# Performance work log

Hardware: AMD Instinct MI355X
Metric: run time of the kernel (lower is better)

## Reference

```python
import jax, jax.numpy as jnp
import numpy as np

FEAT = 256          # feat_channels == point_feat_channels == in_channels
STACK = 3           # stacked_convs
NPTS = 9            # num_points -> dcn_kernel = 3
NCLS = 80           # num_classes
GM = 0.1            # gradient_mul
GROUPS = 32         # 32 * 256 // 256
EPS = 1e-5
BIAS_CLS = -float(np.log((1 - 0.01) / 0.01))  # prior_prob focal-bias init


def conv2d(x, w, b=None):
    y = jax.lax.conv_general_dilated(x, w, (1, 1), 'SAME',
                                     dimension_numbers=('NCHW', 'OIHW', 'NCHW'))
    return y if b is None else y + b[None, :, None, None]


def group_norm(x, w, b):
    B, C, H, W = x.shape
    xg = x.reshape(B, GROUPS, C // GROUPS, H, W)
    mu = xg.mean((2, 3, 4), keepdims=True)
    var = xg.var((2, 3, 4), keepdims=True)
    xn = ((xg - mu) * jax.lax.rsqrt(var + EPS)).reshape(B, C, H, W)
    return xn * w[None, :, None, None] + b[None, :, None, None]


def bilinear_sample(x, py, px):
    # x: [B,C,H,W]; py,px: [B,K,H,W] absolute sample coords -> [B,C,K,H,W]
    B, C, H, W = x.shape
    y0 = jnp.floor(py); x0 = jnp.floor(px)
    wy = (py - y0)[:, None]; wx = (px - x0)[:, None]  # [B,1,K,H,W]
    xf = x.reshape(B, C, H * W)

    def gather(yi, xi):
        valid = (yi >= 0) & (yi < H) & (xi >= 0) & (xi < W)
        yic = jnp.clip(yi, 0, H - 1).astype(jnp.int32)
        xic = jnp.clip(xi, 0, W - 1).astype(jnp.int32)
        idx = (yic * W + xic).reshape(B, -1)                       # [B,K*H*W]
        g = jax.vmap(lambda xb, ib: xb[:, ib])(xf, idx)            # [B,C,K*H*W]
        g = g.reshape(B, C, *yi.shape[1:])
        return g * valid[:, None].astype(x.dtype)

    v00 = gather(y0, x0); v01 = gather(y0, x0 + 1)
    v10 = gather(y0 + 1, x0); v11 = gather(y0 + 1, x0 + 1)
    return (v00 * (1 - wy) * (1 - wx) + v01 * (1 - wy) * wx
            + v10 * wy * (1 - wx) + v11 * wy * wx)


def deform_conv(x, offset, w):
    # x: [B,C,H,W]; offset: [B,2K,H,W] as (dy,dx) per kernel point; w: [O,C,kh,kw]
    B, C, H, W = x.shape
    O, _, kh, kw = w.shape
    K = kh * kw
    off = offset.reshape(B, K, 2, H, W)
    by = jnp.repeat(jnp.arange(kh) - (kh - 1) // 2, kw).astype(x.dtype)  # [K]
    bx = jnp.tile(jnp.arange(kw) - (kw - 1) // 2, kh).astype(x.dtype)
    gy = jnp.arange(H, dtype=x.dtype)[None, None, :, None]
    gx = jnp.arange(W, dtype=x.dtype)[None, None, None, :]
    py = gy + by[None, :, None, None] + off[:, :, 0]  # [B,K,H,W]
    px = gx + bx[None, :, None, None] + off[:, :, 1]
    sampled = bilinear_sample(x, py, px)              # [B,C,K,H,W]
    return jnp.einsum('bckhw,ock->bohw', sampled, w.reshape(O, C, K))


def dcn_base_offset():
    base = np.arange(-1, 2, dtype=np.float32)
    y = np.repeat(base, 3); x = np.tile(base, 3)
    return jnp.asarray(np.stack([y, x], axis=1).reshape(1, -1, 1, 1))  # [1,18,1,1]


def setup_inputs() -> dict:
    key = jax.random.key(0)
    ks = jax.random.split(key, 10)
    std = 0.01
    d = {}
    d['features'] = jax.random.normal(ks[0], (4, FEAT, 64, 64), jnp.float32)
    d['cls_w'] = std * jax.random.normal(ks[1], (STACK, FEAT, FEAT, 3, 3), jnp.float32)
    d['reg_w'] = std * jax.random.normal(ks[2], (STACK, FEAT, FEAT, 3, 3), jnp.float32)
    d['cls_gn_w'] = jnp.ones((STACK, FEAT), jnp.float32)
    d['cls_gn_b'] = jnp.zeros((STACK, FEAT), jnp.float32)
    d['reg_gn_w'] = jnp.ones((STACK, FEAT), jnp.float32)
    d['reg_gn_b'] = jnp.zeros((STACK, FEAT), jnp.float32)
    d['init_conv_w'] = std * jax.random.normal(ks[3], (FEAT, FEAT, 3, 3), jnp.float32)
    d['init_conv_b'] = jnp.zeros((FEAT,), jnp.float32)
    d['init_out_w'] = std * jax.random.normal(ks[4], (2 * NPTS, FEAT, 1, 1), jnp.float32)
    d['init_out_b'] = jnp.zeros((2 * NPTS,), jnp.float32)
    d['cls_dcn_w'] = std * jax.random.normal(ks[5], (FEAT, FEAT, 3, 3), jnp.float32)
    d['cls_out_w'] = std * jax.random.normal(ks[6], (NCLS, FEAT, 1, 1), jnp.float32)
    d['cls_out_b'] = jnp.full((NCLS,), BIAS_CLS, jnp.float32)
    d['ref_dcn_w'] = std * jax.random.normal(ks[7], (FEAT, FEAT, 3, 3), jnp.float32)
    d['ref_out_w'] = std * jax.random.normal(ks[8], (2 * NPTS, FEAT, 1, 1), jnp.float32)
    d['ref_out_b'] = jnp.zeros((2 * NPTS,), jnp.float32)
    return d


def reference(features, cls_w, reg_w, cls_gn_w, cls_gn_b, reg_gn_w, reg_gn_b,
              init_conv_w, init_conv_b, init_out_w, init_out_b,
              cls_dcn_w, cls_out_w, cls_out_b,
              ref_dcn_w, ref_out_w, ref_out_b):
    cls_feat = reg_feat = features
    for i in range(STACK):
        cls_feat = jax.nn.relu(group_norm(conv2d(cls_feat, cls_w[i]), cls_gn_w[i], cls_gn_b[i]))
        reg_feat = jax.nn.relu(group_norm(conv2d(reg_feat, reg_w[i]), reg_gn_w[i], reg_gn_b[i]))
    pts_init = conv2d(jax.nn.relu(conv2d(reg_feat, init_conv_w, init_conv_b)),
                      init_out_w, init_out_b)                     # [B,18,H,W]
    pts_gm = (1.0 - GM) * jax.lax.stop_gradient(pts_init) + GM * pts_init
    dcn_offset = pts_gm - dcn_base_offset()  # DeformConv adds base back internally
    cls_out = conv2d(jax.nn.relu(deform_conv(cls_feat, dcn_offset, cls_dcn_w)),
                     cls_out_w, cls_out_b)                        # [B,80,H,W]
    pts_refine = conv2d(jax.nn.relu(deform_conv(reg_feat, dcn_offset, ref_dcn_w)),
                        ref_out_w, ref_out_b) + jax.lax.stop_gradient(pts_init)
    # outputs concatenated along channels: [cls(80) | pts_init(18) | pts_refine(18)]
    return jnp.concatenate([cls_out, pts_init, pts_refine], axis=1)
```

## Files before the change

kernel.cpp:

```cpp
#include <hip/hip_runtime.h>

typedef unsigned short u16;
typedef unsigned char u8;
typedef __attribute__((ext_vector_type(8))) short short8;
typedef __attribute__((ext_vector_type(4))) float floatx4;
typedef __attribute__((ext_vector_type(2))) float floatx2;
typedef __attribute__((ext_vector_type(2))) long longx2;

#define MTOT    16384
#define PADIMG  (66 * 66)
#define PADELEM (4 * PADIMG * 256)
#define WSTEP   (256 * 2304)

__device__ __forceinline__ float bf2f(u16 u) {
  union { unsigned int i; float f; } c; c.i = ((unsigned int)u) << 16; return c.f;
}
__device__ __forceinline__ u16 f2bf(float f) {
  union { float f; unsigned int i; } c; c.f = f;
  unsigned int r = c.i + 0x7FFFu + ((c.i >> 16) & 1u);
  return (u16)(r >> 16);
}
__device__ __forceinline__ u8 f2fp8(float f) {
  return (u8)(__builtin_amdgcn_cvt_pk_fp8_f32(f, f, 0, false) & 0xFF);
}

__device__ __forceinline__ void gl_lds16(const void* g, void* l) {
  __builtin_amdgcn_global_load_lds(
      (const __attribute__((address_space(1))) void*)g,
      (__attribute__((address_space(3))) void*)l, 16, 0, 0);
}

__device__ __forceinline__ int lds_slot32(int row, int q) {
  return row * 32 + ((q ^ ((row >> 1) & 3)) << 3);
}
__device__ __forceinline__ int permw(int w) {
  return ((w >> 3) & 3) * 16 + ((w >> 5) & 1) * 8 + (w & 7);
}

__global__ void setup_all(const float* __restrict__ cls_w, const float* __restrict__ reg_w,
                          const float* __restrict__ initw, const float* __restrict__ clsd,
                          const float* __restrict__ refd,
                          const float* __restrict__ iw, const float* __restrict__ cw,
                          const float* __restrict__ rw,
                          const float* __restrict__ features,
                          u16* __restrict__ dst1,
                          u8* __restrict__ pads8, u8* __restrict__ wf8) {
  int blk = blockIdx.x;
  int t = threadIdx.x;
  if (blk < 2304) {
    int w = blk >> 8;
    int o = blk & 255;
    const float* src = (w < 3) ? cls_w + (size_t)w * WSTEP
                     : (w < 6) ? reg_w + (size_t)(w - 3) * WSTEP
                     : (w == 6) ? initw : (w == 7) ? clsd : refd;
    __shared__ float wl[2304];
    const float* so = src + (size_t)o * 2304;
    #pragma unroll
    for (int p = 0; p < 9; ++p) wl[p * 256 + t] = so[p * 256 + t];
    __syncthreads();
    if (t < 128) {
      int slot = (w < 6) ? w : (w == 6) ? 8 : (w - 1);
      u8* dw8 = wf8 + (size_t)slot * WSTEP + (size_t)o * 2304;
      int c = 2 * t;
      int pos = (c & 192) + permw(c & 63);
      #pragma unroll
      for (int p = 0; p < 9; ++p) {
        float f0 = wl[c * 9 + p] * 64.f;
        float f1 = wl[(c + 1) * 9 + p] * 64.f;
        int pk = __builtin_amdgcn_cvt_pk_fp8_f32(f0, f1, 0, false);
        *(u16*)(dw8 + p * 256 + pos) = (u16)(pk & 0xFFFF);
      }
    }
  } else if (blk < 2688) {
    int bb = blk - 2304;
    int wsel = bb >> 7;
    const float* src = wsel == 0 ? iw : wsel == 1 ? cw : rw;
    int nvalid = wsel == 1 ? 80 : 18;
    float scale = wsel == 0 ? 1.f : (1.f / 64.f);
    int idx = (bb & 127) * 256 + t;
    int o = idx >> 8, c = idx & 255;
    dst1[(size_t)wsel * 32768 + idx] = f2bf(o < nvalid ? src[o * 256 + c] * scale : 0.f);
  } else if (blk < 3712) {
    __shared__ float tile[64][65];
    int bb = blk - 2688;
    int c0 = (bb & 3) * 64;
    int y  = (bb >> 2) & 63;
    int b  = bb >> 8;
    #pragma unroll
    for (int i = 0; i < 16; ++i) {
      int lin = t + i * 256; int c = lin >> 6, x = lin & 63;
      tile[c][x] = features[((b * 256 + c0 + c) * 64 + y) * 64 + x];
    }
    __syncthreads();
    #pragma unroll
    for (int i = 0; i < 8; ++i) {
      int lin = t + i * 256;
      int x = lin >> 5, c2 = lin & 31;
      int pk = __builtin_amdgcn_cvt_pk_fp8_f32(tile[2 * c2][x], tile[2 * c2 + 1][x], 0, false);
      *(u16*)(pads8 + (size_t)((b * 66 + y + 1) * 66 + (x + 1)) * 256
              + c0 + permw(2 * c2)) = (u16)pk;
    }
  } else {
    int idx = (blk - 3712) * 256 + t;
    int c4 = (idx & 63) << 2;
    int r = idx >> 6;
    int pix = r % 260;
    int ib = r / 260;
    int y, x;
    if (pix < 66)       { y = 0;  x = pix; }
    else if (pix < 132) { y = 65; x = pix - 66; }
    else if (pix < 196) { y = pix - 132 + 1; x = 0; }
    else                { y = pix - 196 + 1; x = 65; }
    size_t o = (((size_t)ib * PADIMG) + y * 66 + x) * 256 + c4;
    *(unsigned int*)(pads8 + o) = 0u;
  }
}

__global__ void __launch_bounds__(256)
gn_apply2(const u8* __restrict__ stage, const float2* __restrict__ st,
          const float* __restrict__ gwc, const float* __restrict__ gbc,
          const float* __restrict__ gwr, const float* __restrict__ gbr,
          u8* __restrict__ cdst8, u8* __restrict__ rdst8) {
  int tid = blockIdx.x * 256 + threadIdx.x;
  int tower = tid >> 20;
  int r = tid & 0xFFFFF;
  int m = r >> 6, c4 = (r & 63) << 2;
  unsigned int v = *(const unsigned int*)(stage + ((size_t)tower << 22)
                                          + (size_t)m * 256 + c4);
  floatx2 lo = __builtin_amdgcn_cvt_pk_f32_fp8(v, false);
  floatx2 hi = __builtin_amdgcn_cvt_pk_f32_fp8(v, true);
  int b = m >> 12, p = m & 4095, y = p >> 6, x = p & 63;
  float2 ss = st[tower * 128 + b * 32 + (c4 >> 3)];
  float mu = ss.x * (1.f / 32768.f);
  float var = ss.y * (1.f / 32768.f) - mu * mu;
  float rinv = rsqrtf(var + 1e-5f);
  const float* gw = tower ? gwr : gwc;
  const float* gb = tower ? gbr : gbc;
  float v0 = fmaxf((lo.x - mu) * rinv * gw[c4 + 0] + gb[c4 + 0], 0.f);
  float v1 = fmaxf((lo.y - mu) * rinv * gw[c4 + 1] + gb[c4 + 1], 0.f);
  float v2 = fmaxf((hi.x - mu) * rinv * gw[c4 + 2] + gb[c4 + 2], 0.f);
  float v3 = fmaxf((hi.y - mu) * rinv * gw[c4 + 3] + gb[c4 + 3], 0.f);
  size_t pixbase = (size_t)((b * 66 + y + 1) * 66 + (x + 1)) * 256;
  int pk = __builtin_amdgcn_cvt_pk_fp8_f32(v0, v1, 0, false);
  pk = __builtin_amdgcn_cvt_pk_fp8_f32(v2, v3, pk, true);
  *(int*)((tower ? rdst8 : cdst8) + pixbase + (c4 & 192) + permw(c4 & 63)) = pk;
}

__global__ void __launch_bounds__(256)
dcn_sample2(const u8* __restrict__ featC, const u8* __restrict__ featR,
            const float* __restrict__ pts,
            u8* __restrict__ AC, u8* __restrict__ AR) {
  int blk = blockIdx.x;
  const u8* featpad = blk < 1024 ? featC : featR;
  u8* A = blk < 1024 ? AC : AR;
  int mblk = blk & 1023;
  int t = threadIdx.x;
  int m = mblk * 16 + (t >> 4);
  int l = t & 15;
  int b = m >> 12, p = m & 4095, y = p >> 6, x = p & 63;
  const float* pp = pts + (size_t)m * 18;
  const u8* fb = featpad + (size_t)b * PADIMG * 256 + l * 4;
  u8* am = A + (size_t)m * 2304 + l * 4;
  #pragma unroll
  for (int kk = 0; kk < 9; ++kk) {
    float py = (float)y + pp[2 * kk];
    float px = (float)x + pp[2 * kk + 1];
    float fy = floorf(py), fx = floorf(px);
    int y0 = (int)fy, x0 = (int)fx;
    float wy = py - fy, wx = px - fx;
    float w00 = (1.f - wy) * (1.f - wx), w01 = (1.f - wy) * wx;
    float w10 = wy * (1.f - wx), w11 = wy * wx;
    bool yok0 = (unsigned)y0 < 64u, yok1 = (unsigned)(y0 + 1) < 64u;
    bool xok0 = (unsigned)x0 < 64u, xok1 = (unsigned)(x0 + 1) < 64u;
    const u8* base = fb + ((y0 + 1) * 66 + (x0 + 1)) * 256;
    float r[16];
    #pragma unroll
    for (int i = 0; i < 16; ++i) r[i] = 0.f;
    #define ACCUM(OFF, W) { \
      _Pragma("unroll") \
      for (int c = 0; c < 4; ++c) { \
        unsigned int v = *(const unsigned int*)(base + (OFF) + c * 64); \
        floatx2 lo = __builtin_amdgcn_cvt_pk_f32_fp8(v, false); \
        floatx2 hi = __builtin_amdgcn_cvt_pk_f32_fp8(v, true); \
        r[c*4+0] += (W) * lo.x; r[c*4+1] += (W) * lo.y; \
        r[c*4+2] += (W) * hi.x; r[c*4+3] += (W) * hi.y; } }
    if (yok0 & xok0) ACCUM(0, w00)
    if (yok0 & xok1) ACCUM(256, w01)
    if (yok1 & xok0) ACCUM(66 * 256, w10)
    if (yok1 & xok1) ACCUM(67 * 256, w11)
    #undef ACCUM
    #pragma unroll
    for (int c = 0; c < 4; ++c) {
      int pk = __builtin_amdgcn_cvt_pk_fp8_f32(r[c*4+0], r[c*4+1], 0, false);
      pk = __builtin_amdgcn_cvt_pk_fp8_f32(r[c*4+2], r[c*4+3], pk, true);
      *(int*)(am + kk * 256 + c * 64) = pk;
    }
  }
}

template <int AMODE, int EP, int KSZ, int BN, int BK, int NPAIR, int FP8 = 0>
__global__ void __launch_bounds__(256)
gemm_kernel(const u16* __restrict__ A0, const u16* __restrict__ A1,
            const u16* __restrict__ W0, const u16* __restrict__ W1,
            const float* __restrict__ bias0, const float* __restrict__ bias1,
            u16* __restrict__ outb0, u16* __restrict__ outb1,
            float2* __restrict__ st0, float2* __restrict__ st1,
            float* __restrict__ outf,
            const float* __restrict__ addpts0, const float* __restrict__ addpts1,
            float* __restrict__ ptsout0, float* __restrict__ ptsout1,
            int nv0, int nv1, int cb0, int cb1) {
  constexpr int NJ = BN / 32;
  constexpr int ABYT = (FP8 == 1) ? 128 * 128 : 128 * BK * 2;
  constexpr int BBYT = (FP8 == 1) ? BN * 128 : BN * BK * 2;
  __shared__ __align__(16) u8 AsB[ABYT];
  __shared__ __align__(16) u8 BsB[BBYT];
  u16* As = (u16*)AsB;
  u16* Bs = (u16*)BsB;
  int t = threadIdx.x;
  int blk = blockIdx.x;
  int pair = 0;
  if constexpr (NPAIR == 2) { pair = blk & 1; blk >>= 1; }
  const u16* A        = pair ? A1 : A0;
  const u16* Wp       = pair ? W1 : W0;
  const float* bias   = pair ? bias1 : bias0;
  u16* outb           = pair ? outb1 : outb0;
  float2* st          = pair ? st1 : st0;
  const float* addpts = pair ? addpts1 : addpts0;
  float* ptsout       = pair ? ptsout1 : ptsout0;
  int nv = pair ? nv1 : nv0;
  int cb = pair ? cb1 : cb0;

  int bm = blk & 127, bn = blk >> 7;
  int lane = t & 63, wave = t >> 6;
  int wm = (wave & 1) << 6;
  int wn = (wave >> 1) * (BN / 2);
  int quad = lane >> 4, r16 = lane & 15;

  floatx4 acc[4][NJ];
  #pragma unroll
  for (int i = 0; i < 4; ++i)
    #pragma unroll
    for (int j = 0; j < NJ; ++j)
      acc[i][j] = (floatx4){0.f, 0.f, 0.f, 0.f};

  if constexpr (FP8 == 1) {
    u8* As8 = AsB;
    u8* Bs8 = BsB;
    const u8* A8 = (const u8*)A;
    const u8* W8 = (const u8*)Wp;
    int sub = t >> 3;
    int cq = (t & 7) ^ (sub & 7);
    int abase[4];
    #pragma unroll
    for (int k = 0; k < 4; ++k) {
      int m = bm * 128 + k * 32 + sub;
      if constexpr (AMODE == 1) {
        int b = m >> 12, p = m & 4095;
        abase[k] = ((b * 66 + (p >> 6)) * 66 + (p & 63)) * 256 + cq * 16;
      } else {
        abase[k] = m * KSZ + cq * 16;
      }
    }
    const u8* wg8 = W8 + (size_t)(bn * BN + sub) * KSZ + cq * 16;

    for (int s = 0; s < KSZ / 128; ++s) {
      int d;
      if constexpr (AMODE == 1) {
        int kk = s >> 1;
        int c0 = (s & 1) << 7;
        int ky = kk / 3, kx = kk - ky * 3;
        d = ((ky * 66 + kx) << 8) + c0;
      } else {
        d = s * 128;
      }
      #pragma unroll
      for (int k = 0; k < 4; ++k)
        gl_lds16(A8 + abase[k] + d, As8 + k * 4096 + t * 16);
      #pragma unroll
      for (int k = 0; k < BN / 32; ++k)
        gl_lds16(wg8 + (size_t)(k * 32) * KSZ + s * 128, Bs8 + k * 4096 + t * 16);
      __syncthreads();
      long af8[2][2][4], bf8[2][2][NJ];
      #pragma unroll
      for (int h = 0; h < 2; ++h) {
        #pragma unroll
        for (int i = 0; i < 4; ++i) {
          int row = wm + i * 16 + r16;
          longx2 v = *(const longx2*)&As8[row * 128 + (((h * 4 + quad) ^ (row & 7)) << 4)];
          af8[h][0][i] = v.x; af8[h][1][i] = v.y;
        }
        #pragma unroll
        for (int j = 0; j < NJ; ++j) {
          int row = wn + j * 16 + r16;
          longx2 v = *(const longx2*)&Bs8[row * 128 + (((h * 4 + quad) ^ (row & 7)) << 4)];
          bf8[h][0][j] = v.x; bf8[h][1][j] = v.y;
        }
      }
      #pragma unroll
      for (int h = 0; h < 2; ++h)
        #pragma unroll
        for (int ks = 0; ks < 2; ++ks)
          #pragma unroll
          for (int i = 0; i < 4; ++i)
            #pragma unroll
            for (int j = 0; j < NJ; ++j)
              acc[i][j] = __builtin_amdgcn_mfma_f32_16x16x32_fp8_fp8(
                  af8[h][ks][i], bf8[h][ks][j], acc[i][j], 0, 0, 0);
      __syncthreads();
    }
  } else {
    int row = t >> 2;
    int chunkS = (t & 3) ^ ((t >> 3) & 3);
    int m0 = bm * 128 + row, m1 = m0 + 64;
    int abase0, abase1;
    if constexpr (AMODE == 1) {
      int b0 = m0 >> 12, p0 = m0 & 4095;
      int b1 = m1 >> 12, p1 = m1 & 4095;
      abase0 = ((b0 * 66 + (p0 >> 6)) * 66 + (p0 & 63)) * 256 + chunkS * 8;
      abase1 = ((b1 * 66 + (p1 >> 6)) * 66 + (p1 & 63)) * 256 + chunkS * 8;
    } else {
      abase0 = m0 * KSZ + chunkS * 8;
      abase1 = m1 * KSZ + chunkS * 8;
    }
    const u16* wg = Wp + (size_t)(bn * BN + row) * KSZ + chunkS * 8;

    for (int s = 0; s < KSZ / 32; ++s) {
      int d;
      if constexpr (AMODE == 1) {
        int kk = s >> 3;
        int c0 = (s & 7) << 5;
        int ky = kk / 3, kx = kk - ky * 3;
        d = ((ky * 66 + kx) << 8) + c0;
      } else {
        d = s * 32;
      }
      gl_lds16(A + abase0 + d, &As[t * 8]);
      gl_lds16(A + abase1 + d, &As[2048 + t * 8]);
      gl_lds16(wg + s * 32, &Bs[t * 8]);
      if constexpr (BN == 128)
        gl_lds16(wg + (size_t)64 * KSZ + s * 32, &Bs[2048 + t * 8]);
      __syncthreads();
      short8 af[4], bfr[NJ];
      #pragma unroll
      for (int i = 0; i < 4; ++i)
        af[i] = *(const short8*)&As[lds_slot32(wm + i * 16 + r16, quad)];
      #pragma unroll
      for (int j = 0; j < NJ; ++j)
        bfr[j] = *(const short8*)&Bs[lds_slot32(wn + j * 16 + r16, quad)];
      #pragma unroll
      for (int i = 0; i < 4; ++i)
        #pragma unroll
        for (int j = 0; j < NJ; ++j)
          acc[i][j] = __builtin_amdgcn_mfma_f32_16x16x32_bf16(af[i], bfr[j], acc[i][j], 0, 0, 0);
      __syncthreads();
    }
  }

  #pragma unroll
  for (int j = 0; j < NJ; ++j) {
    int gn = bn * BN + wn + j * 16 + r16;
    float s = 0.f, s2 = 0.f;
    #pragma unroll
    for (int i = 0; i < 4; ++i) {
      #pragma unroll
      for (int r = 0; r < 4; ++r) {
        int gm = bm * 128 + wm + i * 16 + quad * 4 + r;
        float v = acc[i][j][r];
        if constexpr (EP == 0) {
          ((u8*)outb)[(size_t)gm * 256 + gn] = f2fp8(v);
          s += v; s2 += v * v;
        } else if constexpr (EP == 1) {
          if constexpr (FP8 == 1) v *= (1.f / 64.f);
          outb[(size_t)gm * 256 + gn] = f2bf(fmaxf(v + bias[gn], 0.f));
        } else if constexpr (EP == 2) {
          outb[(size_t)gm * 256 + gn] = f2bf(fmaxf(v, 0.f));
        } else {
          if (gn < nv) {
            v += bias[gn];
            if (addpts) v += addpts[(size_t)gm * 18 + gn];
            if (ptsout) ptsout[(size_t)gm * 18 + gn] = v;
            int bb = gm >> 12, p = gm & 4095;
            outf[(size_t)((bb * 116 + cb + gn) << 12) + p] = v;
          }
        }
      }
    }
    if constexpr (EP == 0) {
      s += __shfl_xor(s, 1);  s2 += __shfl_xor(s2, 1);
      s += __shfl_xor(s, 2);  s2 += __shfl_xor(s2, 2);
      s += __shfl_xor(s, 4);  s2 += __shfl_xor(s2, 4);
      s += __shfl_xor(s, 16); s2 += __shfl_xor(s2, 16);
      s += __shfl_xor(s, 32); s2 += __shfl_xor(s2, 32);
      if ((lane & 55) == 0) {
        float2* sp = st + ((bm >> 5) * 32) + (gn >> 3);
        atomicAdd(&sp->x, s);
        atomicAdd(&sp->y, s2);
      }
    }
  }
}

extern "C" void kernel_launch(void* const* d_in, const int* in_sizes, int n_in,
                              void* d_out, int out_size, void* d_ws, size_t ws_size,
                              hipStream_t stream) {
  (void)in_sizes; (void)n_in; (void)out_size;
  const float* features    = (const float*)d_in[0];
  const float* cls_w       = (const float*)d_in[1];
  const float* reg_w       = (const float*)d_in[2];
  const float* cls_gn_w    = (const float*)d_in[3];
  const float* cls_gn_b    = (const float*)d_in[4];
  const float* reg_gn_w    = (const float*)d_in[5];
  const float* reg_gn_b    = (const float*)d_in[6];
  const float* init_conv_w = (const float*)d_in[7];
  const float* init_conv_b = (const float*)d_in[8];
  const float* init_out_w  = (const float*)d_in[9];
  const float* init_out_b  = (const float*)d_in[10];
  const float* cls_dcn_w   = (const float*)d_in[11];
  const float* cls_out_w   = (const float*)d_in[12];
  const float* cls_out_b   = (const float*)d_in[13];
  const float* ref_dcn_w   = (const float*)d_in[14];
  const float* ref_out_w   = (const float*)d_in[15];
  const float* ref_out_b   = (const float*)d_in[16];
  float* out = (float*)d_out;

  char* ws = (char*)d_ws;
  size_t off = 0;
  auto alloc = [&](size_t bytes) {
    char* p = ws + off;
    off += (bytes + 255) & ~(size_t)255;
    return p;
  };
  u8*  wf8        = (u8*)alloc((size_t)9 * WSTEP);
  u16* w1         = (u16*)alloc((size_t)3 * 32768 * 2);
  u8* xpad8       = (u8*)alloc(PADELEM);
  u8* cpadA8      = (u8*)alloc(PADELEM);
  u8* cpadB8      = (u8*)alloc(PADELEM);
  u8* rpadA8      = (u8*)alloc(PADELEM);
  u8* rpadB8      = (u8*)alloc(PADELEM);
  float* ptsbuf   = (float*)alloc((size_t)MTOT * 18 * 4);
  float2* statsAll= (float2*)alloc(3 * 256 * sizeof(float2));
  u16* initf      = (u16*)alloc((size_t)MTOT * 256 * 2);
  u16* dcnout     = (u16*)alloc((size_t)2 * MTOT * 256 * 2);
  char* unionReg  = alloc((size_t)MTOT * 2304);
  u8* cstage8     = (u8*)unionReg;
  u8* adcn        = (u8*)unionReg;
  u8* adcn2       = (u8*)alloc((size_t)MTOT * 2304);
  bool paired_dcn = (off <= ws_size);

  (void)hipMemsetAsync(statsAll, 0, 3 * 256 * sizeof(float2), stream);
  setup_all<<<5012, 256, 0, stream>>>(cls_w, reg_w, init_conv_w, cls_dcn_w, ref_dcn_w,
                                      init_out_w, cls_out_w, ref_out_w, features,
                                      w1, xpad8, wf8);

  const u8* curC = xpad8; const u8* curR = xpad8;
  u8* nxtC = cpadA8; u8* altC = cpadB8;
  u8* nxtR = rpadA8; u8* altR = rpadB8;
  for (int i = 0; i < 3; ++i) {
    gemm_kernel<1, 0, 2304, 64, 128, 2, 1><<<1024, 256, 0, stream>>>(
        (const u16*)curC, (const u16*)curR,
        (const u16*)(wf8 + (size_t)i * WSTEP), (const u16*)(wf8 + (size_t)(3 + i) * WSTEP),
        nullptr, nullptr, (u16*)cstage8, (u16*)(cstage8 + (size_t)MTOT * 256),
        statsAll + i * 256, statsAll + i * 256 + 128,
        nullptr, nullptr, nullptr, nullptr, nullptr, 0, 0, 0, 0);
    gn_apply2<<<8192, 256, 0, stream>>>(cstage8, statsAll + i * 256,
        cls_gn_w + i * 256, cls_gn_b + i * 256, reg_gn_w + i * 256, reg_gn_b + i * 256,
        nxtC, nxtR);
    curC = nxtC; { u8* tmp = nxtC; nxtC = altC; altC = tmp; }
    curR = nxtR; { u8* tmp = nxtR; nxtR = altR; altR = tmp; }
  }
  const u8* cls_feat8 = curC;
  const u8* reg_feat8 = curR;

  gemm_kernel<1, 1, 2304, 32, 128, 1, 1><<<1024, 256, 0, stream>>>(
      (const u16*)reg_feat8, nullptr, (const u16*)(wf8 + (size_t)8 * WSTEP), nullptr,
      init_conv_b, nullptr, initf, nullptr, nullptr, nullptr,
      nullptr, nullptr, nullptr, nullptr, nullptr, 0, 0, 0, 0);
  gemm_kernel<0, 3, 256, 64, 32, 1><<<256, 256, 0, stream>>>(
      initf, nullptr, w1, nullptr, init_out_b, nullptr,
      nullptr, nullptr, nullptr, nullptr, out,
      nullptr, nullptr, ptsbuf, nullptr, 18, 0, 80, 0);

  if (paired_dcn) {
    dcn_sample2<<<2048, 256, 0, stream>>>(cls_feat8, reg_feat8, ptsbuf, adcn, adcn2);
    gemm_kernel<0, 2, 2304, 64, 128, 2, 1><<<1024, 256, 0, stream>>>(
        (const u16*)adcn, (const u16*)adcn2,
        (const u16*)(wf8 + (size_t)6 * WSTEP), (const u16*)(wf8 + (size_t)7 * WSTEP),
        nullptr, nullptr, dcnout, dcnout + (size_t)MTOT * 256, nullptr, nullptr,
        nullptr, nullptr, nullptr, nullptr, nullptr, 0, 0, 0, 0);
  } else {
    dcn_sample2<<<1024, 256, 0, stream>>>(cls_feat8, cls_feat8, ptsbuf, adcn, adcn);
    gemm_kernel<0, 2, 2304, 64, 128, 1, 1><<<512, 256, 0, stream>>>(
        (const u16*)adcn, nullptr, (const u16*)(wf8 + (size_t)6 * WSTEP), nullptr,
        nullptr, nullptr, dcnout, nullptr, nullptr, nullptr,
        nullptr, nullptr, nullptr, nullptr, nullptr, 0, 0, 0, 0);
    dcn_sample2<<<1024, 256, 0, stream>>>(reg_feat8, reg_feat8, ptsbuf, adcn, adcn);
    gemm_kernel<0, 2, 2304, 64, 128, 1, 1><<<512, 256, 0, stream>>>(
        (const u16*)adcn, nullptr, (const u16*)(wf8 + (size_t)7 * WSTEP), nullptr,
        nullptr, nullptr, dcnout + (size_t)MTOT * 256, nullptr, nullptr, nullptr,
        nullptr, nullptr, nullptr, nullptr, nullptr, 0, 0, 0, 0);
  }

  gemm_kernel<0, 3, 256, 64, 32, 2><<<512, 256, 0, stream>>>(
      dcnout, dcnout + (size_t)MTOT * 256, w1 + 32768, w1 + 2 * 32768,
      cls_out_b, ref_out_b, nullptr, nullptr, nullptr, nullptr, out,
      nullptr, ptsbuf, nullptr, nullptr, 80, 18, 0, 98);
}
```

Measured before the change: 352.7 us.

## Move 1x1 output convs and intermediates to FP8 and vectorize DCN sampling

The intermediate activations (init conv features and deform-conv outputs) are now stored as FP8 in the permuted channel layout instead of bf16. The 1x1 output convolutions switch to the FP8 GEMM path, with their weights prescaled by 64 and a compile-time right-shift rescale in the epilogue. The DCN sampler now does one 16-byte load and one 16-byte store per corner, instead of four 4-byte accesses. Together these cut memory traffic and move the small GEMMs onto FP8 matrix cores, at the cost of extra quantization error in the point outputs.

```diff
diff --git a/kernel.cpp b/kernel.cpp
--- a/kernel.cpp
+++ b/kernel.cpp
@@ -6,6 +6,7 @@
 typedef __attribute__((ext_vector_type(4))) float floatx4;
 typedef __attribute__((ext_vector_type(2))) float floatx2;
 typedef __attribute__((ext_vector_type(2))) long longx2;
+typedef __attribute__((ext_vector_type(4))) unsigned int uintx4;
 
 #define MTOT    16384
 #define PADIMG  (66 * 66)
@@ -35,6 +36,9 @@
 }
 __device__ __forceinline__ int permw(int w) {
   return ((w >> 3) & 3) * 16 + ((w >> 5) & 1) * 8 + (w & 7);
+}
+__device__ __forceinline__ int permc(int c) {
+  return (c & 192) + permw(c & 63);
 }
 
 __global__ void setup_all(const float* __restrict__ cls_w, const float* __restrict__ reg_w,
@@ -43,7 +47,7 @@
                           const float* __restrict__ iw, const float* __restrict__ cw,
                           const float* __restrict__ rw,
                           const float* __restrict__ features,
-                          u16* __restrict__ dst1,
+                          u8* __restrict__ wf1,
                           u8* __restrict__ pads8, u8* __restrict__ wf8) {
   int blk = blockIdx.x;
   int t = threadIdx.x;
@@ -62,7 +66,7 @@
       int slot = (w < 6) ? w : (w == 6) ? 8 : (w - 1);
       u8* dw8 = wf8 + (size_t)slot * WSTEP + (size_t)o * 2304;
       int c = 2 * t;
-      int pos = (c & 192) + permw(c & 63);
+      int pos = permc(c);
       #pragma unroll
       for (int p = 0; p < 9; ++p) {
         float f0 = wl[c * 9 + p] * 64.f;
@@ -76,10 +80,9 @@
     int wsel = bb >> 7;
     const float* src = wsel == 0 ? iw : wsel == 1 ? cw : rw;
     int nvalid = wsel == 1 ? 80 : 18;
-    float scale = wsel == 0 ? 1.f : (1.f / 64.f);
-    int idx = (bb & 127) * 256 + t;
-    int o = idx >> 8, c = idx & 255;
-    dst1[(size_t)wsel * 32768 + idx] = f2bf(o < nvalid ? src[o * 256 + c] * scale : 0.f);
+    int o = bb & 127;
+    float v = (o < nvalid) ? src[o * 256 + t] * 64.f : 0.f;
+    wf1[(size_t)wsel * 32768 + o * 256 + permc(t)] = f2fp8(v);
   } else if (blk < 3712) {
     __shared__ float tile[64][65];
     int bb = blk - 2688;
@@ -143,7 +146,7 @@
   size_t pixbase = (size_t)((b * 66 + y + 1) * 66 + (x + 1)) * 256;
   int pk = __builtin_amdgcn_cvt_pk_fp8_f32(v0, v1, 0, false);
   pk = __builtin_amdgcn_cvt_pk_fp8_f32(v2, v3, pk, true);
-  *(int*)((tower ? rdst8 : cdst8) + pixbase + (c4 & 192) + permw(c4 & 63)) = pk;
+  *(int*)((tower ? rdst8 : cdst8) + pixbase + permc(c4)) = pk;
 }
 
 __global__ void __launch_bounds__(256)
@@ -159,8 +162,8 @@
   int l = t & 15;
   int b = m >> 12, p = m & 4095, y = p >> 6, x = p & 63;
   const float* pp = pts + (size_t)m * 18;
-  const u8* fb = featpad + (size_t)b * PADIMG * 256 + l * 4;
-  u8* am = A + (size_t)m * 2304 + l * 4;
+  const u8* fb = featpad + (size_t)b * PADIMG * 256 + l * 16;
+  u8* am = A + (size_t)m * 2304 + l * 16;
   #pragma unroll
   for (int kk = 0; kk < 9; ++kk) {
     float py = (float)y + pp[2 * kk];
@@ -177,28 +180,30 @@
     #pragma unroll
     for (int i = 0; i < 16; ++i) r[i] = 0.f;
     #define ACCUM(OFF, W) { \
+      uintx4 v = *(const uintx4*)(base + (OFF)); \
       _Pragma("unroll") \
-      for (int c = 0; c < 4; ++c) { \
-        unsigned int v = *(const unsigned int*)(base + (OFF) + c * 64); \
-        floatx2 lo = __builtin_amdgcn_cvt_pk_f32_fp8(v, false); \
-        floatx2 hi = __builtin_amdgcn_cvt_pk_f32_fp8(v, true); \
-        r[c*4+0] += (W) * lo.x; r[c*4+1] += (W) * lo.y; \
-        r[c*4+2] += (W) * hi.x; r[c*4+3] += (W) * hi.y; } }
+      for (int e = 0; e < 4; ++e) { \
+        floatx2 lo = __builtin_amdgcn_cvt_pk_f32_fp8(v[e], false); \
+        floatx2 hi = __builtin_amdgcn_cvt_pk_f32_fp8(v[e], true); \
+        r[e*4+0] += (W) * lo.x; r[e*4+1] += (W) * lo.y; \
+        r[e*4+2] += (W) * hi.x; r[e*4+3] += (W) * hi.y; } }
     if (yok0 & xok0) ACCUM(0, w00)
     if (yok0 & xok1) ACCUM(256, w01)
     if (yok1 & xok0) ACCUM(66 * 256, w10)
     if (yok1 & xok1) ACCUM(67 * 256, w11)
     #undef ACCUM
-    #pragma unroll
-    for (int c = 0; c < 4; ++c) {
-      int pk = __builtin_amdgcn_cvt_pk_fp8_f32(r[c*4+0], r[c*4+1], 0, false);
-      pk = __builtin_amdgcn_cvt_pk_fp8_f32(r[c*4+2], r[c*4+3], pk, true);
-      *(int*)(am + kk * 256 + c * 64) = pk;
-    }
+    uintx4 o4;
+    #pragma unroll
+    for (int e = 0; e < 4; ++e) {
+      int pk = __builtin_amdgcn_cvt_pk_fp8_f32(r[e*4+0], r[e*4+1], 0, false);
+      pk = __builtin_amdgcn_cvt_pk_fp8_f32(r[e*4+2], r[e*4+3], pk, true);
+      o4[e] = (unsigned int)pk;
+    }
+    *(uintx4*)(am + kk * 256) = o4;
   }
 }
 
-template <int AMODE, int EP, int KSZ, int BN, int BK, int NPAIR, int FP8 = 0>
+template <int AMODE, int EP, int KSZ, int BN, int BK, int NPAIR, int FP8 = 0, int RSH = 0>
 __global__ void __launch_bounds__(256)
 gemm_kernel(const u16* __restrict__ A0, const u16* __restrict__ A1,
             const u16* __restrict__ W0, const u16* __restrict__ W1,
@@ -356,6 +361,7 @@
     }
   }
 
+  constexpr float RS = 1.f / (float)(1 << RSH);
   #pragma unroll
   for (int j = 0; j < NJ; ++j) {
     int gn = bn * BN + wn + j * 16 + r16;
@@ -370,12 +376,21 @@
           ((u8*)outb)[(size_t)gm * 256 + gn] = f2fp8(v);
           s += v; s2 += v * v;
         } else if constexpr (EP == 1) {
-          if constexpr (FP8 == 1) v *= (1.f / 64.f);
-          outb[(size_t)gm * 256 + gn] = f2bf(fmaxf(v + bias[gn], 0.f));
+          if constexpr (RSH > 0) v *= RS;
+          float o = fmaxf(v + bias[gn], 0.f);
+          if constexpr (FP8 == 1)
+            ((u8*)outb)[(size_t)gm * 256 + permc(gn)] = f2fp8(o);
+          else
+            outb[(size_t)gm * 256 + gn] = f2bf(o);
         } else if constexpr (EP == 2) {
-          outb[(size_t)gm * 256 + gn] = f2bf(fmaxf(v, 0.f));
+          float o = fmaxf(v, 0.f);
+          if constexpr (FP8 == 1)
+            ((u8*)outb)[(size_t)gm * 256 + permc(gn)] = f2fp8(o);
+          else
+            outb[(size_t)gm * 256 + gn] = f2bf(o);
         } else {
           if (gn < nv) {
+            if constexpr (RSH > 0) v *= RS;
             v += bias[gn];
             if (addpts) v += addpts[(size_t)gm * 18 + gn];
             if (ptsout) ptsout[(size_t)gm * 18 + gn] = v;
@@ -431,7 +446,7 @@
     return p;
   };
   u8*  wf8        = (u8*)alloc((size_t)9 * WSTEP);
-  u16* w1         = (u16*)alloc((size_t)3 * 32768 * 2);
+  u8*  wf1        = (u8*)alloc((size_t)3 * 32768);
   u8* xpad8       = (u8*)alloc(PADELEM);
   u8* cpadA8      = (u8*)alloc(PADELEM);
   u8* cpadB8      = (u8*)alloc(PADELEM);
@@ -439,8 +454,8 @@
   u8* rpadB8      = (u8*)alloc(PADELEM);
   float* ptsbuf   = (float*)alloc((size_t)MTOT * 18 * 4);
   float2* statsAll= (float2*)alloc(3 * 256 * sizeof(float2));
-  u16* initf      = (u16*)alloc((size_t)MTOT * 256 * 2);
-  u16* dcnout     = (u16*)alloc((size_t)2 * MTOT * 256 * 2);
+  u8* initf       = (u8*)alloc((size_t)MTOT * 256);
+  u8* dcnout      = (u8*)alloc((size_t)2 * MTOT * 256);
   char* unionReg  = alloc((size_t)MTOT * 2304);
   u8* cstage8     = (u8*)unionReg;
   u8* adcn        = (u8*)unionReg;
@@ -450,7 +465,7 @@
   (void)hipMemsetAsync(statsAll, 0, 3 * 256 * sizeof(float2), stream);
   setup_all<<<5012, 256, 0, stream>>>(cls_w, reg_w, init_conv_w, cls_dcn_w, ref_dcn_w,
                                       init_out_w, cls_out_w, ref_out_w, features,
-                                      w1, xpad8, wf8);
+                                      wf1, xpad8, wf8);
 
   const u8* curC = xpad8; const u8* curR = xpad8;
   u8* nxtC = cpadA8; u8* altC = cpadB8;
@@ -471,13 +486,13 @@
   const u8* cls_feat8 = curC;
   const u8* reg_feat8 = curR;
 
-  gemm_kernel<1, 1, 2304, 32, 128, 1, 1><<<1024, 256, 0, stream>>>(
+  gemm_kernel<1, 1, 2304, 32, 128, 1, 1, 6><<<1024, 256, 0, stream>>>(
       (const u16*)reg_feat8, nullptr, (const u16*)(wf8 + (size_t)8 * WSTEP), nullptr,
-      init_conv_b, nullptr, initf, nullptr, nullptr, nullptr,
+      init_conv_b, nullptr, (u16*)initf, nullptr, nullptr, nullptr,
       nullptr, nullptr, nullptr, nullptr, nullptr, 0, 0, 0, 0);
-  gemm_kernel<0, 3, 256, 64, 32, 1><<<256, 256, 0, stream>>>(
-      initf, nullptr, w1, nullptr, init_out_b, nullptr,
-      nullptr, nullptr, nullptr, nullptr, out,
+  gemm_kernel<0, 3, 256, 32, 128, 1, 1, 6><<<512, 256, 0, stream>>>(
+      (const u16*)initf, nullptr, (const u16*)wf1, nullptr,
+      init_out_b, nullptr, nullptr, nullptr, nullptr, nullptr, out,
       nullptr, nullptr, ptsbuf, nullptr, 18, 0, 80, 0);
 
   if (paired_dcn) {
@@ -485,23 +500,24 @@
     gemm_kernel<0, 2, 2304, 64, 128, 2, 1><<<1024, 256, 0, stream>>>(
         (const u16*)adcn, (const u16*)adcn2,
         (const u16*)(wf8 + (size_t)6 * WSTEP), (const u16*)(wf8 + (size_t)7 * WSTEP),
-        nullptr, nullptr, dcnout, dcnout + (size_t)MTOT * 256, nullptr, nullptr,
+        nullptr, nullptr, (u16*)dcnout, (u16*)(dcnout + (size_t)MTOT * 256), nullptr, nullptr,
         nullptr, nullptr, nullptr, nullptr, nullptr, 0, 0, 0, 0);
   } else {
     dcn_sample2<<<1024, 256, 0, stream>>>(cls_feat8, cls_feat8, ptsbuf, adcn, adcn);
     gemm_kernel<0, 2, 2304, 64, 128, 1, 1><<<512, 256, 0, stream>>>(
         (const u16*)adcn, nullptr, (const u16*)(wf8 + (size_t)6 * WSTEP), nullptr,
-        nullptr, nullptr, dcnout, nullptr, nullptr, nullptr,
+        nullptr, nullptr, (u16*)dcnout, nullptr, nullptr, nullptr,
         nullptr, nullptr, nullptr, nullptr, nullptr, 0, 0, 0, 0);
     dcn_sample2<<<1024, 256, 0, stream>>>(reg_feat8, reg_feat8, ptsbuf, adcn, adcn);
     gemm_kernel<0, 2, 2304, 64, 128, 1, 1><<<512, 256, 0, stream>>>(
         (const u16*)adcn, nullptr, (const u16*)(wf8 + (size_t)7 * WSTEP), nullptr,
-        nullptr, nullptr, dcnout + (size_t)MTOT * 256, nullptr, nullptr, nullptr,
+        nullptr, nullptr, (u16*)(dcnout + (size_t)MTOT * 256), nullptr, nullptr, nullptr,
         nullptr, nullptr, nullptr, nullptr, nullptr, 0, 0, 0, 0);
   }
 
-  gemm_kernel<0, 3, 256, 64, 32, 2><<<512, 256, 0, stream>>>(
-      dcnout, dcnout + (size_t)MTOT * 256, w1 + 32768, w1 + 2 * 32768,
+  gemm_kernel<0, 3, 256, 32, 128, 2, 1, 12><<<1024, 256, 0, stream>>>(
+      (const u16*)dcnout, (const u16*)(dcnout + (size_t)MTOT * 256),
+      (const u16*)(wf1 + 32768), (const u16*)(wf1 + 65536),
       cls_out_b, ref_out_b, nullptr, nullptr, nullptr, nullptr, out,
       nullptr, ptsbuf, nullptr, nullptr, 80, 18, 0, 98);
 }
```

Result: faster. 335.2 us (-5.0%).
